# Performance work log

Measured on AMD Instinct MI355X. Metric: run time of the kernel, lower is better.

## Reference

```python
import jax, jax.numpy as jnp
import numpy as np

E, T, IN, OUT = 8, 16384, 1024, 1024  # n_groups, total_tokens, in_features, out_features


def setup_inputs() -> dict:
    key = jax.random.key(0)
    kx, kw, ks = jax.random.split(key, 3)
    x = jax.random.normal(kx, (T, IN), dtype=jnp.float32)
    # kaiming_uniform-ish scale for weight [E, OUT, IN]
    weight = jax.random.normal(kw, (E, OUT, IN), dtype=jnp.float32) * (1.0 / np.sqrt(IN))
    # ragged segment lengths that sum exactly to T (random cut points)
    cuts = jnp.sort(jax.random.randint(ks, (E - 1,), 0, T + 1)).astype(jnp.int32)
    seg_lens = jnp.diff(
        jnp.concatenate([jnp.zeros((1,), jnp.int32), cuts, jnp.full((1,), T, jnp.int32)])
    )
    return {"x": x, "weight": weight, "seg_lens": seg_lens}


def reference(x, weight, seg_lens):
    # Grouped GEMM: row t of x is multiplied by weight[g(t)].T where g(t) is the
    # segment (expert) that token t falls into per seg_lens. trans_b=True.
    n_groups = weight.shape[0]
    bounds = jnp.cumsum(seg_lens)                                  # [E]
    seg_id = jnp.searchsorted(bounds, jnp.arange(x.shape[0]), side="right")  # [T]
    y = jnp.zeros((x.shape[0], weight.shape[1]), dtype=x.dtype)
    for e in range(n_groups):  # small fixed loop over groups
        y = y + jnp.where((seg_id == e)[:, None], x @ weight[e].T, 0)
    return y
```

## Files before the change

### kernel.cpp

```cpp
#include <hip/hip_runtime.h>

#define T_TOK  16384
#define IN_F   1024
#define OUT_F  1024
#define NE     8

typedef __bf16 bf16;
typedef bf16  bf16x4 __attribute__((ext_vector_type(4)));
typedef bf16  bf16x8 __attribute__((ext_vector_type(8)));
typedef float f32x4  __attribute__((ext_vector_type(4)));

#define CVT_THREADS 256
#define NX_CHUNKS (T_TOK * IN_F / 4)
#define NW_CHUNKS (NE * OUT_F * IN_F / 4)
#define NO_CHUNKS (T_TOK * OUT_F / 4)
#define NCVT_CHUNKS (NX_CHUNKS + NW_CHUNKS)
#define NALL_CHUNKS (NCVT_CHUNKS + NO_CHUNKS)

__global__ __launch_bounds__(CVT_THREADS)
void cvt_and_zero(const float* __restrict__ x, const float* __restrict__ w,
                  bf16* __restrict__ xb, bf16* __restrict__ wb,
                  float* __restrict__ out)
{
    for (int i = blockIdx.x * CVT_THREADS + threadIdx.x; i < NALL_CHUNKS;
         i += gridDim.x * CVT_THREADS) {
        if (i < NCVT_CHUNKS) {
            const bool isx = (i < NX_CHUNKS);
            const int  j   = isx ? i : i - NX_CHUNKS;
            f32x4 v = isx ? ((const f32x4*)x)[j] : ((const f32x4*)w)[j];
            bf16x4 h;
            #pragma unroll
            for (int k = 0; k < 4; ++k) h[k] = (bf16)v[k];
            if (isx) ((bf16x4*)xb)[j] = h;
            else     ((bf16x4*)wb)[j] = h;
        } else {
            f32x4 z = {0.f, 0.f, 0.f, 0.f};
            ((f32x4*)out)[i - NCVT_CHUNKS] = z;
        }
    }
}

#define BM 256
#define BN 256
#define BK 64
#define GTHREADS 512
#define NBLOCKS 256
#define KCH (IN_F / BK)

__device__ __forceinline__ void gld_lds16(const bf16* g, bf16* l) {
    __builtin_amdgcn_global_load_lds(
        (const __attribute__((address_space(1))) void*)g,
        (__attribute__((address_space(3))) void*)l,
        16, 0, 0);
}

__device__ __forceinline__ void resolve_slot(const int* sl, int slot,
                                             int& e_sel, int& row0, int& rows)
{
    e_sel = -1; row0 = 0; rows = 0;
    int start = 0, acct = 0;
    #pragma unroll
    for (int e = 0; e < NE; ++e) {
        int len = sl[e];
        int nt  = (len + BM - 1) >> 8;
        if (e_sel < 0 && slot >= acct && slot < acct + nt) {
            e_sel = e;
            row0  = start + (slot - acct) * BM;
            int rm = start + len - row0;
            rows = rm < BM ? rm : BM;
        }
        acct  += nt;
        start += len;
    }
}

__global__ __launch_bounds__(GTHREADS)
void grouped_gemm_main(const bf16* __restrict__ xb,
                       const bf16* __restrict__ wb,
                       const int*  __restrict__ seg_lens,
                       float* __restrict__ out)
{
    __shared__ __align__(16) bf16 As[2][BM * BK];
    __shared__ __align__(16) bf16 Bs[2][BN * BK];

    const int tile = blockIdx.x;
    const int slot = tile >> 2;
    const int col0 = (tile & 3) << 8;

    int sl[NE];
    #pragma unroll
    for (int e = 0; e < NE; ++e) sl[e] = seg_lens[e];

    int e_sel, row0, rows;
    resolve_slot(sl, slot, e_sel, row0, rows);
    if (e_sel < 0) return;

    const int tid  = threadIdx.x;
    const int lane = tid & 63;
    const int wave = tid >> 6;
    const int wr   = wave >> 2;
    const int wc   = wave & 3;
    const int quad = lane >> 4;
    const int l16  = lane & 15;
    const int rq   = lane >> 3;
    const int ke   = (lane & 7) * 8;
    const int q0   = wave * 4;

    const bf16* wbase = wb + ((size_t)e_sel * OUT_F + (size_t)col0) * IN_F;

    const bf16* ga[4];
    const bf16* gb[4];
    #pragma unroll
    for (int i = 0; i < 4; ++i) {
        int q  = wave * 4 + i;
        int ra = row0 + q * 8 + rq;
        if (ra > T_TOK - 1) ra = T_TOK - 1;
        ga[i] = xb + (size_t)ra * IN_F + ke;
        gb[i] = wbase + (size_t)(q * 8 + rq) * IN_F + ke;
    }

    f32x4 acc[8][4] = {};

    #pragma unroll
    for (int i = 0; i < 4; ++i) {
        gld_lds16(ga[i], &As[0][(q0 + i) * 512]);
        gld_lds16(gb[i], &Bs[0][(q0 + i) * 512]);
    }
    __syncthreads();

    int cur = 0;
    for (int ks = 0; ks < KCH; ++ks) {
        const int kn = (ks + 1) * BK;
        if (kn < IN_F) {
            #pragma unroll
            for (int i = 0; i < 4; ++i) {
                gld_lds16(ga[i] + kn, &As[cur ^ 1][(q0 + i) * 512]);
                gld_lds16(gb[i] + kn, &Bs[cur ^ 1][(q0 + i) * 512]);
            }
        }

        #pragma unroll
        for (int kk = 0; kk < 2; ++kk) {
            bf16x8 af[8], bfr[4];
            #pragma unroll
            for (int t = 0; t < 8; ++t)
                af[t] = *(const bf16x8*)(
                    &As[cur][(wr * 128 + t * 16 + l16) * BK + kk * 32 + quad * 8]);
            #pragma unroll
            for (int v = 0; v < 4; ++v)
                bfr[v] = *(const bf16x8*)(
                    &Bs[cur][(wc * 64 + v * 16 + l16) * BK + kk * 32 + quad * 8]);
            #pragma unroll
            for (int t = 0; t < 8; ++t)
                #pragma unroll
                for (int v = 0; v < 4; ++v)
                    acc[t][v] = __builtin_amdgcn_mfma_f32_16x16x32_bf16(
                        af[t], bfr[v], acc[t][v], 0, 0, 0);
        }

        __syncthreads();
        cur ^= 1;
    }

    #pragma unroll
    for (int t = 0; t < 8; ++t) {
        #pragma unroll
        for (int r = 0; r < 4; ++r) {
            int row = wr * 128 + t * 16 + quad * 4 + r;
            if (row < rows) {
                size_t ob = (size_t)(row0 + row) * OUT_F + col0 + wc * 64;
                #pragma unroll
                for (int v = 0; v < 4; ++v)
                    out[ob + v * 16 + l16] = acc[t][v][r];
            }
        }
    }
}

__global__ __launch_bounds__(GTHREADS)
void grouped_gemm_surplus(const bf16* __restrict__ xb,
                          const bf16* __restrict__ wb,
                          const int*  __restrict__ seg_lens,
                          float* __restrict__ out)
{
    __shared__ __align__(16) bf16 As[2][BM * BK];
    __shared__ __align__(16) bf16 Bs[2][BN * BK];

    const int tid  = threadIdx.x;
    const int lane = tid & 63;
    const int wave = tid >> 6;
    const int wr   = wave >> 2;
    const int wc   = wave & 3;
    const int quad = lane >> 4;
    const int l16  = lane & 15;
    const int rq   = lane >> 3;
    const int ke   = (lane & 7) * 8;
    const int q0   = wave * 4;
    const int b    = blockIdx.x;

    int sl[NE];
    #pragma unroll
    for (int e = 0; e < NE; ++e) sl[e] = seg_lens[e];

    int n_slots = 0;
    #pragma unroll
    for (int e = 0; e < NE; ++e) n_slots += (sl[e] + BM - 1) >> 8;
    const int L = n_slots * (OUT_F / BN);

    const int Uleft = (L - NBLOCKS) * KCH;
    if (Uleft <= 0) return;

    const int base = Uleft >> 8;
    const int rem  = Uleft & 255;
    int u    = NBLOCKS * KCH + b * base + (b < rem ? b : rem);
    int uend = u + base + (b < rem ? 1 : 0);

    while (u < uend) {
        const int tile = u >> 4;
        const int kc0  = u & (KCH - 1);
        int kc1 = kc0 + (uend - u);
        if (kc1 > KCH) kc1 = KCH;
        u += kc1 - kc0;

        const int slot = tile >> 2;
        const int col0 = (tile & 3) << 8;
        int e_sel, row0, rows;
        resolve_slot(sl, slot, e_sel, row0, rows);

        const bf16* wbase = wb + ((size_t)e_sel * OUT_F + (size_t)col0) * IN_F;

        const bf16* ga[4];
        const bf16* gb[4];
        #pragma unroll
        for (int i = 0; i < 4; ++i) {
            int q  = wave * 4 + i;
            int ra = row0 + q * 8 + rq;
            if (ra > T_TOK - 1) ra = T_TOK - 1;
            ga[i] = xb + (size_t)ra * IN_F + ke;
            gb[i] = wbase + (size_t)(q * 8 + rq) * IN_F + ke;
        }

        f32x4 acc[8][4] = {};

        {
            const int kb = kc0 * BK;
            #pragma unroll
            for (int i = 0; i < 4; ++i) {
                gld_lds16(ga[i] + kb, &As[0][(q0 + i) * 512]);
                gld_lds16(gb[i] + kb, &Bs[0][(q0 + i) * 512]);
            }
        }
        __syncthreads();

        int cur = 0;
        for (int ks = kc0; ks < kc1; ++ks) {
            const int kn = (ks + 1) * BK;
            if (ks + 1 < kc1) {
                #pragma unroll
                for (int i = 0; i < 4; ++i) {
                    gld_lds16(ga[i] + kn, &As[cur ^ 1][(q0 + i) * 512]);
                    gld_lds16(gb[i] + kn, &Bs[cur ^ 1][(q0 + i) * 512]);
                }
            }

            #pragma unroll
            for (int kk = 0; kk < 2; ++kk) {
                bf16x8 af[8], bfr[4];
                #pragma unroll
                for (int t = 0; t < 8; ++t)
                    af[t] = *(const bf16x8*)(
                        &As[cur][(wr * 128 + t * 16 + l16) * BK + kk * 32 + quad * 8]);
                #pragma unroll
                for (int v = 0; v < 4; ++v)
                    bfr[v] = *(const bf16x8*)(
                        &Bs[cur][(wc * 64 + v * 16 + l16) * BK + kk * 32 + quad * 8]);
                #pragma unroll
                for (int t = 0; t < 8; ++t)
                    #pragma unroll
                    for (int v = 0; v < 4; ++v)
                        acc[t][v] = __builtin_amdgcn_mfma_f32_16x16x32_bf16(
                            af[t], bfr[v], acc[t][v], 0, 0, 0);
            }

            __syncthreads();
            cur ^= 1;
        }

        #pragma unroll
        for (int t = 0; t < 8; ++t) {
            #pragma unroll
            for (int r = 0; r < 4; ++r) {
                int row = wr * 128 + t * 16 + quad * 4 + r;
                if (row < rows) {
                    size_t ob = (size_t)(row0 + row) * OUT_F + col0 + wc * 64;
                    #pragma unroll
                    for (int v = 0; v < 4; ++v)
                        unsafeAtomicAdd(&out[ob + v * 16 + l16], acc[t][v][r]);
                }
            }
        }
    }
}

#define FBM 128
#define FBK 32
#define FTHREADS 256
#define FROW_SLOTS 136

__global__ __launch_bounds__(FTHREADS)
void grouped_gemm_f32io_bf16(const float* __restrict__ x,
                             const float* __restrict__ wgt,
                             const int*  __restrict__ seg_lens,
                             float* __restrict__ out)
{
    __shared__ __align__(16) bf16 Asf[FBM * FBK];
    __shared__ __align__(16) bf16 Bsf[FBM * FBK];

    const int m    = blockIdx.y;
    const int col0 = blockIdx.x * FBM;

    int e_sel = -1, row0 = 0, rows = 0;
    {
        int start = 0, acct = 0;
        #pragma unroll
        for (int e = 0; e < NE; ++e) {
            int len = seg_lens[e];
            int nt  = (len + FBM - 1) >> 7;
            if (e_sel < 0 && m >= acct && m < acct + nt) {
                e_sel = e;
                row0  = start + (m - acct) * FBM;
                int rem = start + len - row0;
                rows = rem < FBM ? rem : FBM;
            }
            acct  += nt;
            start += len;
        }
    }
    if (e_sel < 0) return;

    const int tid  = threadIdx.x;
    const int lane = tid & 63;
    const int wave = tid >> 6;
    const int wm   = (wave >> 1) * 64;
    const int wn   = (wave & 1) * 64;
    const int quad = lane >> 4;
    const int l16  = lane & 15;

    const float* wbase = wgt + ((size_t)e_sel * OUT_F + (size_t)col0) * IN_F;

    f32x4 acc[4][4] = {};

    for (int k0 = 0; k0 < IN_F; k0 += FBK) {
        f32x4 a_st[4], b_st[4];
        #pragma unroll
        for (int t = 0; t < 4; ++t) {
            int c  = t * FTHREADS + tid;
            int rg = row0 + (c >> 3);
            if (rg > T_TOK - 1) rg = T_TOK - 1;
            a_st[t] = *(const f32x4*)(x + (size_t)rg * IN_F + k0 + (c & 7) * 4);
            b_st[t] = *(const f32x4*)(wbase + (size_t)(c >> 3) * IN_F + k0 + (c & 7) * 4);
        }

        __syncthreads();

        #pragma unroll
        for (int t = 0; t < 4; ++t) {
            int c = t * FTHREADS + tid;
            bf16x4 ha, hb;
            #pragma unroll
            for (int j = 0; j < 4; ++j) { ha[j] = (bf16)a_st[t][j]; hb[j] = (bf16)b_st[t][j]; }
            *(bf16x4*)(&Asf[(c >> 3) * FBK + (c & 7) * 4]) = ha;
            *(bf16x4*)(&Bsf[(c >> 3) * FBK + (c & 7) * 4]) = hb;
        }
        __syncthreads();

        bf16x8 af[4], bfr[4];
        #pragma unroll
        for (int t = 0; t < 4; ++t)
            af[t] = *(const bf16x8*)(&Asf[(wm + t * 16 + l16) * FBK + quad * 8]);
        #pragma unroll
        for (int v = 0; v < 4; ++v)
            bfr[v] = *(const bf16x8*)(&Bsf[(wn + v * 16 + l16) * FBK + quad * 8]);

        #pragma unroll
        for (int t = 0; t < 4; ++t)
            #pragma unroll
            for (int v = 0; v < 4; ++v)
                acc[t][v] = __builtin_amdgcn_mfma_f32_16x16x32_bf16(
                    af[t], bfr[v], acc[t][v], 0, 0, 0);
    }

    #pragma unroll
    for (int t = 0; t < 4; ++t) {
        #pragma unroll
        for (int r = 0; r < 4; ++r) {
            int row = wm + t * 16 + quad * 4 + r;
            if (row < rows) {
                size_t ob = (size_t)(row0 + row) * OUT_F + col0;
                #pragma unroll
                for (int v = 0; v < 4; ++v)
                    out[ob + wn + v * 16 + l16] = acc[t][v][r];
            }
        }
    }
}

extern "C" void kernel_launch(void* const* d_in, const int* in_sizes, int n_in,
                              void* d_out, int out_size, void* d_ws, size_t ws_size,
                              hipStream_t stream) {
    const float* x   = (const float*)d_in[0];
    const float* wgt = (const float*)d_in[1];
    const int*   seg = (const int*)d_in[2];
    float* out = (float*)d_out;

    const size_t xbytes = (size_t)T_TOK * IN_F * sizeof(bf16);
    const size_t wbytes = (size_t)NE * OUT_F * IN_F * sizeof(bf16);

    if (ws_size >= xbytes + wbytes) {
        bf16* xb = (bf16*)d_ws;
        bf16* wb = (bf16*)((char*)d_ws + xbytes);
        cvt_and_zero<<<dim3(2048, 1, 1), dim3(CVT_THREADS, 1, 1), 0, stream>>>(
            x, wgt, xb, wb, out);
        grouped_gemm_main<<<dim3(NBLOCKS, 1, 1), dim3(GTHREADS, 1, 1), 0, stream>>>(
            xb, wb, seg, out);
        grouped_gemm_surplus<<<dim3(NBLOCKS, 1, 1), dim3(GTHREADS, 1, 1), 0, stream>>>(
            xb, wb, seg, out);
    } else {
        grouped_gemm_f32io_bf16<<<dim3(OUT_F / FBM, FROW_SLOTS, 1),
                                  dim3(FTHREADS, 1, 1), 0, stream>>>(x, wgt, seg, out);
    }
}
```

Measured before the change: 236.8 us.

## Split surplus tiles into fixed 4-way K slices and zero only surplus output rows

The surplus kernel now gives each block one tile and one quarter of K (4 of 16 chunks), launched as 112 blocks, instead of spreading stream-K work ranges across 256 blocks. The conversion kernel now zeroes only the output rows covered by surplus tiles (from the row where slot 64 starts), assuming the main kernel fully writes the earlier rows. This cuts redundant zero-fill traffic and simplifies the surplus scheduling. The risks are correctness if the number of surplus tiles exceeds 28, and uneven load balance under the fixed split.

Result: faster. 215.0 us (-9.2%).

```diff
diff --git a/kernel.cpp b/kernel.cpp
--- a/kernel.cpp
+++ b/kernel.cpp
@@ -10,19 +10,43 @@
 typedef bf16  bf16x8 __attribute__((ext_vector_type(8)));
 typedef float f32x4  __attribute__((ext_vector_type(4)));
 
+#define BM 256
+#define BN 256
+#define BK 64
+#define GTHREADS 512
+#define NBLOCKS 256
+#define KCH (IN_F / BK)
+#define SP_BLOCKS 112
+
 #define CVT_THREADS 256
 #define NX_CHUNKS (T_TOK * IN_F / 4)
 #define NW_CHUNKS (NE * OUT_F * IN_F / 4)
-#define NO_CHUNKS (T_TOK * OUT_F / 4)
 #define NCVT_CHUNKS (NX_CHUNKS + NW_CHUNKS)
-#define NALL_CHUNKS (NCVT_CHUNKS + NO_CHUNKS)
 
 __global__ __launch_bounds__(CVT_THREADS)
 void cvt_and_zero(const float* __restrict__ x, const float* __restrict__ w,
                   bf16* __restrict__ xb, bf16* __restrict__ wb,
-                  float* __restrict__ out)
+                  const int* __restrict__ seg_lens, float* __restrict__ out)
 {
-    for (int i = blockIdx.x * CVT_THREADS + threadIdx.x; i < NALL_CHUNKS;
+    int r64 = T_TOK;
+    {
+        int slots = 0, start = 0;
+        #pragma unroll
+        for (int e = 0; e < NE; ++e) {
+            int len = seg_lens[e];
+            int nt  = (len + BM - 1) >> 8;
+            if (slots <= 64 && slots + nt > 64) {
+                r64 = start + (64 - slots) * BM;
+            }
+            slots += nt;
+            start += len;
+        }
+    }
+    const int zero_chunks = (T_TOK - r64) * (OUT_F / 4);
+    const int zbase       = r64 * (OUT_F / 4);
+    const int tot         = NCVT_CHUNKS + zero_chunks;
+
+    for (int i = blockIdx.x * CVT_THREADS + threadIdx.x; i < tot;
          i += gridDim.x * CVT_THREADS) {
         if (i < NCVT_CHUNKS) {
             const bool isx = (i < NX_CHUNKS);
@@ -35,17 +59,10 @@
             else     ((bf16x4*)wb)[j] = h;
         } else {
             f32x4 z = {0.f, 0.f, 0.f, 0.f};
-            ((f32x4*)out)[i - NCVT_CHUNKS] = z;
-        }
-    }
-}
-
-#define BM 256
-#define BN 256
-#define BK 64
-#define GTHREADS 512
-#define NBLOCKS 256
-#define KCH (IN_F / BK)
+            ((f32x4*)out)[zbase + (i - NCVT_CHUNKS)] = z;
+        }
+    }
+}
 
 __device__ __forceinline__ void gld_lds16(const bf16* g, bf16* l) {
     __builtin_amdgcn_global_load_lds(
@@ -186,6 +203,24 @@
     __shared__ __align__(16) bf16 As[2][BM * BK];
     __shared__ __align__(16) bf16 Bs[2][BN * BK];
 
+    const int tile   = NBLOCKS + (blockIdx.x >> 2);
+    const int kslice = blockIdx.x & 3;
+
+    int sl[NE];
+    #pragma unroll
+    for (int e = 0; e < NE; ++e) sl[e] = seg_lens[e];
+
+    int n_slots = 0;
+    #pragma unroll
+    for (int e = 0; e < NE; ++e) n_slots += (sl[e] + BM - 1) >> 8;
+    const int L = n_slots * (OUT_F / BN);
+    if (tile >= L) return;
+
+    const int slot = tile >> 2;
+    const int col0 = (tile & 3) << 8;
+    int e_sel, row0, rows;
+    resolve_slot(sl, slot, e_sel, row0, rows);
+
     const int tid  = threadIdx.x;
     const int lane = tid & 63;
     const int wave = tid >> 6;
@@ -196,107 +231,75 @@
     const int rq   = lane >> 3;
     const int ke   = (lane & 7) * 8;
     const int q0   = wave * 4;
-    const int b    = blockIdx.x;
-
-    int sl[NE];
-    #pragma unroll
-    for (int e = 0; e < NE; ++e) sl[e] = seg_lens[e];
-
-    int n_slots = 0;
-    #pragma unroll
-    for (int e = 0; e < NE; ++e) n_slots += (sl[e] + BM - 1) >> 8;
-    const int L = n_slots * (OUT_F / BN);
-
-    const int Uleft = (L - NBLOCKS) * KCH;
-    if (Uleft <= 0) return;
-
-    const int base = Uleft >> 8;
-    const int rem  = Uleft & 255;
-    int u    = NBLOCKS * KCH + b * base + (b < rem ? b : rem);
-    int uend = u + base + (b < rem ? 1 : 0);
-
-    while (u < uend) {
-        const int tile = u >> 4;
-        const int kc0  = u & (KCH - 1);
-        int kc1 = kc0 + (uend - u);
-        if (kc1 > KCH) kc1 = KCH;
-        u += kc1 - kc0;
-
-        const int slot = tile >> 2;
-        const int col0 = (tile & 3) << 8;
-        int e_sel, row0, rows;
-        resolve_slot(sl, slot, e_sel, row0, rows);
-
-        const bf16* wbase = wb + ((size_t)e_sel * OUT_F + (size_t)col0) * IN_F;
-
-        const bf16* ga[4];
-        const bf16* gb[4];
-        #pragma unroll
-        for (int i = 0; i < 4; ++i) {
-            int q  = wave * 4 + i;
-            int ra = row0 + q * 8 + rq;
-            if (ra > T_TOK - 1) ra = T_TOK - 1;
-            ga[i] = xb + (size_t)ra * IN_F + ke;
-            gb[i] = wbase + (size_t)(q * 8 + rq) * IN_F + ke;
-        }
-
-        f32x4 acc[8][4] = {};
-
-        {
-            const int kb = kc0 * BK;
+
+    const bf16* wbase = wb + ((size_t)e_sel * OUT_F + (size_t)col0) * IN_F;
+
+    const bf16* ga[4];
+    const bf16* gb[4];
+    #pragma unroll
+    for (int i = 0; i < 4; ++i) {
+        int q  = wave * 4 + i;
+        int ra = row0 + q * 8 + rq;
+        if (ra > T_TOK - 1) ra = T_TOK - 1;
+        ga[i] = xb + (size_t)ra * IN_F + ke;
+        gb[i] = wbase + (size_t)(q * 8 + rq) * IN_F + ke;
+    }
+
+    f32x4 acc[8][4] = {};
+
+    const int kb0 = kslice * 4 * BK;
+
+    #pragma unroll
+    for (int i = 0; i < 4; ++i) {
+        gld_lds16(ga[i] + kb0, &As[0][(q0 + i) * 512]);
+        gld_lds16(gb[i] + kb0, &Bs[0][(q0 + i) * 512]);
+    }
+    __syncthreads();
+
+    #pragma unroll
+    for (int j = 0; j < 4; ++j) {
+        const int cur = j & 1;
+        if (j < 3) {
+            const int kn = kb0 + (j + 1) * BK;
             #pragma unroll
             for (int i = 0; i < 4; ++i) {
-                gld_lds16(ga[i] + kb, &As[0][(q0 + i) * 512]);
-                gld_lds16(gb[i] + kb, &Bs[0][(q0 + i) * 512]);
-            }
-        }
-        __syncthreads();
-
-        int cur = 0;
-        for (int ks = kc0; ks < kc1; ++ks) {
-            const int kn = (ks + 1) * BK;
-            if (ks + 1 < kc1) {
-                #pragma unroll
-                for (int i = 0; i < 4; ++i) {
-                    gld_lds16(ga[i] + kn, &As[cur ^ 1][(q0 + i) * 512]);
-                    gld_lds16(gb[i] + kn, &Bs[cur ^ 1][(q0 + i) * 512]);
-                }
-            }
-
-            #pragma unroll
-            for (int kk = 0; kk < 2; ++kk) {
-                bf16x8 af[8], bfr[4];
-                #pragma unroll
-                for (int t = 0; t < 8; ++t)
-                    af[t] = *(const bf16x8*)(
-                        &As[cur][(wr * 128 + t * 16 + l16) * BK + kk * 32 + quad * 8]);
+                gld_lds16(ga[i] + kn, &As[cur ^ 1][(q0 + i) * 512]);
+                gld_lds16(gb[i] + kn, &Bs[cur ^ 1][(q0 + i) * 512]);
+            }
+        }
+
+        #pragma unroll
+        for (int kk = 0; kk < 2; ++kk) {
+            bf16x8 af[8], bfr[4];
+            #pragma unroll
+            for (int t = 0; t < 8; ++t)
+                af[t] = *(const bf16x8*)(
+                    &As[cur][(wr * 128 + t * 16 + l16) * BK + kk * 32 + quad * 8]);
+            #pragma unroll
+            for (int v = 0; v < 4; ++v)
+                bfr[v] = *(const bf16x8*)(
+                    &Bs[cur][(wc * 64 + v * 16 + l16) * BK + kk * 32 + quad * 8]);
+            #pragma unroll
+            for (int t = 0; t < 8; ++t)
                 #pragma unroll
                 for (int v = 0; v < 4; ++v)
-                    bfr[v] = *(const bf16x8*)(
-                        &Bs[cur][(wc * 64 + v * 16 + l16) * BK + kk * 32 + quad * 8]);
+                    acc[t][v] = __builtin_amdgcn_mfma_f32_16x16x32_bf16(
+                        af[t], bfr[v], acc[t][v], 0, 0, 0);
+        }
+
+        __syncthreads();
+    }
+
+    #pragma unroll
+    for (int t = 0; t < 8; ++t) {
+        #pragma unroll
+        for (int r = 0; r < 4; ++r) {
+            int row = wr * 128 + t * 16 + quad * 4 + r;
+            if (row < rows) {
+                size_t ob = (size_t)(row0 + row) * OUT_F + col0 + wc * 64;
                 #pragma unroll
-                for (int t = 0; t < 8; ++t)
-                    #pragma unroll
-                    for (int v = 0; v < 4; ++v)
-                        acc[t][v] = __builtin_amdgcn_mfma_f32_16x16x32_bf16(
-                            af[t], bfr[v], acc[t][v], 0, 0, 0);
-            }
-
-            __syncthreads();
-            cur ^= 1;
-        }
-
-        #pragma unroll
-        for (int t = 0; t < 8; ++t) {
-            #pragma unroll
-            for (int r = 0; r < 4; ++r) {
-                int row = wr * 128 + t * 16 + quad * 4 + r;
-                if (row < rows) {
-                    size_t ob = (size_t)(row0 + row) * OUT_F + col0 + wc * 64;
-                    #pragma unroll
-                    for (int v = 0; v < 4; ++v)
-                        unsafeAtomicAdd(&out[ob + v * 16 + l16], acc[t][v][r]);
-                }
+                for (int v = 0; v < 4; ++v)
+                    unsafeAtomicAdd(&out[ob + v * 16 + l16], acc[t][v][r]);
             }
         }
     }
@@ -420,10 +423,10 @@
         bf16* xb = (bf16*)d_ws;
         bf16* wb = (bf16*)((char*)d_ws + xbytes);
         cvt_and_zero<<<dim3(2048, 1, 1), dim3(CVT_THREADS, 1, 1), 0, stream>>>(
-            x, wgt, xb, wb, out);
+            x, wgt, xb, wb, seg, out);
         grouped_gemm_main<<<dim3(NBLOCKS, 1, 1), dim3(GTHREADS, 1, 1), 0, stream>>>(
             xb, wb, seg, out);
-        grouped_gemm_surplus<<<dim3(NBLOCKS, 1, 1), dim3(GTHREADS, 1, 1), 0, stream>>>(
+        grouped_gemm_surplus<<<dim3(SP_BLOCKS, 1, 1), dim3(GTHREADS, 1, 1), 0, stream>>>(
             xb, wb, seg, out);
     } else {
         grouped_gemm_f32io_bf16<<<dim3(OUT_F / FBM, FROW_SLOTS, 1),
```
